# Kernel optimization log

Measured on AMD Instinct MI355X. Metric: run time of the kernel, lower is better.

The kernel has to match this reference:

```python
import jax, jax.numpy as jnp
import numpy as np

B, D, TC, TE, TGT = 8, 256, 2048, 2048, 256
SCALE = 16.0  # sqrt(256.0) hardcoded in the original module


def setup_inputs() -> dict:
    key = jax.random.key(0)
    k1, k2, k3 = jax.random.split(key, 3)
    content_emb = jax.random.normal(k1, (B, D, TC), dtype=jnp.float32)
    emotion_emb = jax.random.normal(k2, (B, D, TE), dtype=jnp.float32)
    # Conv1d(embed_dim*2 -> target_embed, kernel=3): weight [out, in, k]
    fan_in = 2 * D * 3
    conv_w = jax.random.normal(k3, (TGT, 2 * D, 3), dtype=jnp.float32) / np.sqrt(fan_in)
    conv_b = jnp.zeros((TGT,), dtype=jnp.float32)
    return {"content_emb": content_emb, "emotion_emb": emotion_emb,
            "conv_w": conv_w, "conv_b": conv_b}


def reference(content_emb, emotion_emb, conv_w, conv_b):
    # (B, D, T) -> (B, T, D)
    c = jnp.transpose(content_emb, (0, 2, 1))   # [B, Tc, D]
    e = jnp.transpose(emotion_emb, (0, 2, 1))   # [B, Te, D]
    sim = jnp.einsum('btd,bsd->bts', c, e)      # [B, Tc, Te]
    attn = jax.nn.softmax(sim / SCALE, axis=-1)
    weighted_emo = jnp.einsum('bts,bsd->btd', attn, e)  # [B, Tc, D]
    x = jnp.concatenate([c, weighted_emo], axis=-1)     # [B, Tc, 2D]
    x = jnp.transpose(x, (0, 2, 1))                     # [B, 2D, Tc]
    out = jax.lax.conv_general_dilated(
        x, conv_w, window_strides=(1,), padding=[(1, 1)],
        dimension_numbers=('NCH', 'OIH', 'NCH'))
    return out + conv_b[None, :, None]
```

## Files before the change

### kernel.cpp

```cpp
#include <hip/hip_runtime.h>

typedef __bf16 bf16x8 __attribute__((ext_vector_type(8)));
typedef __bf16 bf16x4 __attribute__((ext_vector_type(4)));
typedef float  f32x4  __attribute__((ext_vector_type(4)));

#define MFMA(a, b, c) __builtin_amdgcn_mfma_f32_16x16x32_bf16((a), (b), (c), 0, 0, 0)
#define DRAIN_VMCNT() __builtin_amdgcn_s_waitcnt(0x0F70)

constexpr int Bc  = 8;
constexpr int D   = 256;
constexpr int TC  = 2048;
constexpr int TE  = 2048;
constexpr int TGT = 256;
constexpr int XR  = 512;
constexpr int CROW = 520;
constexpr int NBT = Bc * TC;

#define EXP_C 0.09016844005556021f

__device__ __forceinline__ void gl_lds16(const __bf16* g, __bf16* l) {
  __builtin_amdgcn_global_load_lds(
      (const __attribute__((address_space(1))) void*)g,
      (__attribute__((address_space(3))) void*)l, 16, 0, 0);
}

__global__ void k_transpose_f(const float* __restrict__ src, __bf16* __restrict__ dst,
                              int T, int rowStride) {
  __shared__ __bf16 tile[64][68];
  const int b  = blockIdx.z;
  const int t0 = blockIdx.x * 64;
  const int d0 = blockIdx.y * 64;
  const int tid = threadIdx.x;
  const int c4 = (tid & 15) * 4;
  const int r0 = tid >> 4;
  const float* sp = src + ((size_t)b * D + d0) * T + t0;
#pragma unroll
  for (int i = 0; i < 4; ++i) {
    const int r = r0 + 16 * i;
    const float4 v = *(const float4*)(sp + (size_t)r * T + c4);
    bf16x4 wv;
    wv[0] = (__bf16)v.x; wv[1] = (__bf16)v.y; wv[2] = (__bf16)v.z; wv[3] = (__bf16)v.w;
    *(bf16x4*)&tile[r][c4] = wv;
  }
  __syncthreads();
  __bf16* dp = dst + ((size_t)b * T + t0) * rowStride + d0;
#pragma unroll
  for (int i = 0; i < 2; ++i) {
    const int idx = tid + 256 * i;
    const int r   = idx >> 3;
    const int c8  = (idx & 7) * 8;
    bf16x8 v;
#pragma unroll
    for (int j = 0; j < 8; ++j) v[j] = tile[c8 + j][r];
    *(bf16x8*)(dp + (size_t)r * rowStride + c8) = v;
  }
}

__global__ void k_prep_emo(const float* __restrict__ src, __bf16* __restrict__ e_t,
                           __bf16* __restrict__ e_ds) {
  __shared__ __bf16 tile[64][68];
  const int b  = blockIdx.z;
  const int t0 = blockIdx.x * 64;
  const int d0 = blockIdx.y * 64;
  const int tid = threadIdx.x;
  const int c4 = (tid & 15) * 4;
  const int r0 = tid >> 4;
  const float* sp = src + ((size_t)b * D + d0) * TE + t0;
  __bf16* dsp = e_ds + ((size_t)b * D + d0) * TE + t0;
#pragma unroll
  for (int i = 0; i < 4; ++i) {
    const int r = r0 + 16 * i;
    const float4 v = *(const float4*)(sp + (size_t)r * TE + c4);
    bf16x4 wv;
    wv[0] = (__bf16)v.x; wv[1] = (__bf16)v.y; wv[2] = (__bf16)v.z; wv[3] = (__bf16)v.w;
    *(bf16x4*)&tile[r][c4] = wv;
    *(bf16x4*)(dsp + (size_t)r * TE + c4) = wv;
  }
  __syncthreads();
  __bf16* dp = e_t + ((size_t)b * TE + t0) * D + d0;
#pragma unroll
  for (int i = 0; i < 2; ++i) {
    const int idx = tid + 256 * i;
    const int r   = idx >> 3;
    const int c8  = (idx & 7) * 8;
    bf16x8 v;
#pragma unroll
    for (int j = 0; j < 8; ++j) v[j] = tile[c8 + j][r];
    *(bf16x8*)(dp + (size_t)r * D + c8) = v;
  }
}

__global__ void k_wpack_f(const float* __restrict__ w, __bf16* __restrict__ Wk) {
  const int idx = blockIdx.x * 256 + threadIdx.x;
  const int o = idx >> 9, i = idx & 511;
#pragma unroll
  for (int k = 0; k < 3; ++k)
    Wk[k * (TGT * 512) + idx] = (__bf16)w[(size_t)o * 1536 + i * 3 + k];
}

__global__ __launch_bounds__(256, 2) void k_attn(const __bf16* __restrict__ xcat,
                                                 const __bf16* __restrict__ e_t,
                                                 const __bf16* __restrict__ e_ds,
                                                 __bf16* __restrict__ Op,
                                                 float* __restrict__ Lp) {
  __shared__ __align__(16) __bf16 sEt[2][8192];
  __shared__ __align__(16) __bf16 sEs[2][8192];
  __shared__ __align__(16) __bf16 sP[4][2][640];

  const int tid  = threadIdx.x;
  const int lane = tid & 63;
  const int w    = tid >> 6;
  const int q    = lane >> 4;
  const int tl   = lane & 15;
  const int b    = blockIdx.y;
  const int z    = blockIdx.z;
  const int tbase = blockIdx.x * 128 + w * 32;

  const __bf16* etb = e_t  + (size_t)b * TE * D;
  const __bf16* esb = e_ds + (size_t)b * D * TE;

  bf16x8 cB[2][8];
#pragma unroll
  for (int tt = 0; tt < 2; ++tt) {
    const __bf16* crow = xcat + ((size_t)(b * TC) + tbase + tt * 16 + tl) * XR + q * 8;
#pragma unroll
    for (int ks = 0; ks < 8; ++ks) cB[tt][ks] = *(const bf16x8*)(crow + ks * 32);
  }

  unsigned offEt[4], offEs[4];
#pragma unroll
  for (int c = 0; c < 4; ++c) {
    const int id = (w * 4 + c) * 64 + lane;
    const int ss = id >> 5, cs = id & 31;
    offEt[c] = ss * D + (cs ^ (ss & 7)) * 8;
    const int dd = id >> 2, ps = id & 3;
    offEs[c] = dd * TE + (ps ^ ((dd >> 2) & 3)) * 8;
  }

  f32x4 accO[2][16];
#pragma unroll
  for (int tt = 0; tt < 2; ++tt)
#pragma unroll
    for (int dt = 0; dt < 16; ++dt) accO[tt][dt] = (f32x4){0.f, 0.f, 0.f, 0.f};
  float lacc[2] = {0.f, 0.f};

  const int sbase = z * (TE / 4);
  const int sw3 = (tl >> 2) & 3;

  auto stage = [&](int buf, int s0) {
#pragma unroll
    for (int c = 0; c < 4; ++c) {
      gl_lds16(etb + (size_t)s0 * D + offEt[c], &sEt[buf][(w * 4 + c) * 512]);
      gl_lds16(esb + s0 + offEs[c], &sEs[buf][(w * 4 + c) * 512]);
    }
  };

  stage(0, sbase);
  DRAIN_VMCNT();
  __syncthreads();

  int cur = 0;
  for (int k = 0; k < TE / 128; ++k) {
    if (k < TE / 128 - 1) stage(cur ^ 1, sbase + (k + 1) * 32);

    f32x4 aS[2][2];
#pragma unroll
    for (int i = 0; i < 2; ++i)
#pragma unroll
      for (int j = 0; j < 2; ++j) aS[i][j] = (f32x4){0.f, 0.f, 0.f, 0.f};
    const __bf16* pe = &sEt[cur][0];
    __builtin_amdgcn_s_setprio(1);
#pragma unroll
    for (int ks = 0; ks < 8; ++ks) {
      const int ch = (ks * 4 + q) ^ (tl & 7);
      bf16x8 a0 = *(const bf16x8*)(pe + (tl * 32 + ch) * 8);
      bf16x8 a1 = *(const bf16x8*)(pe + ((16 + tl) * 32 + ch) * 8);
      aS[0][0] = MFMA(a0, cB[0][ks], aS[0][0]);
      aS[0][1] = MFMA(a0, cB[1][ks], aS[0][1]);
      aS[1][0] = MFMA(a1, cB[0][ks], aS[1][0]);
      aS[1][1] = MFMA(a1, cB[1][ks], aS[1][1]);
    }
    __builtin_amdgcn_s_setprio(0);

#pragma unroll
    for (int tt = 0; tt < 2; ++tt) {
      bf16x4 w0, w1;
#pragma unroll
      for (int r = 0; r < 4; ++r) {
        float e0 = exp2f(aS[0][tt][r] * EXP_C);
        float e1 = exp2f(aS[1][tt][r] * EXP_C);
        lacc[tt] += e0 + e1;
        w0[r] = (__bf16)e0;
        w1[r] = (__bf16)e1;
      }
      __bf16* pw = &sP[w][tt][tl * 40 + q * 4];
      *(bf16x4*)pw = w0;
      *(bf16x4*)(pw + 16) = w1;
    }
    bf16x8 pB0 = *(const bf16x8*)(&sP[w][0][tl * 40 + q * 8]);
    bf16x8 pB1 = *(const bf16x8*)(&sP[w][1][tl * 40 + q * 8]);

    const __bf16* ps = &sEs[cur][0];
    __builtin_amdgcn_s_setprio(1);
#pragma unroll
    for (int dt = 0; dt < 16; ++dt) {
      bf16x8 a = *(const bf16x8*)(ps + ((dt * 16 + tl) * 4 + (q ^ sw3)) * 8);
      accO[0][dt] = MFMA(a, pB0, accO[0][dt]);
      accO[1][dt] = MFMA(a, pB1, accO[1][dt]);
    }
    __builtin_amdgcn_s_setprio(0);

    DRAIN_VMCNT();
    __syncthreads();
    cur ^= 1;
  }

#pragma unroll
  for (int tt = 0; tt < 2; ++tt) {
    float v = lacc[tt];
    v += __shfl_xor(v, 16, 64);
    v += __shfl_xor(v, 32, 64);
    const size_t row = (size_t)z * NBT + b * TC + tbase + tt * 16 + tl;
    if (q == 0) Lp[row] = v;
    __bf16* orow = Op + row * D + q * 4;
#pragma unroll
    for (int dt = 0; dt < 16; ++dt) {
      bf16x4 o;
#pragma unroll
      for (int r = 0; r < 4; ++r) o[r] = (__bf16)accO[tt][dt][r];
      *(bf16x4*)(orow + dt * 16) = o;
    }
  }
}

__global__ void k_norm(const __bf16* __restrict__ Op, const float* __restrict__ Lp,
                       __bf16* __restrict__ xcat) {
  const int row  = blockIdx.x * 4 + (threadIdx.x >> 6);
  const int lane = threadIdx.x & 63;
  float lsum = 0.f;
#pragma unroll
  for (int zz = 0; zz < 4; ++zz) lsum += Lp[zz * NBT + row];
  const float inv = 1.0f / lsum;
  float acc[4] = {0.f, 0.f, 0.f, 0.f};
#pragma unroll
  for (int zz = 0; zz < 4; ++zz) {
    bf16x4 a = *(const bf16x4*)(Op + ((size_t)zz * NBT + row) * D + lane * 4);
#pragma unroll
    for (int r = 0; r < 4; ++r) acc[r] += (float)a[r];
  }
  bf16x4 o;
#pragma unroll
  for (int r = 0; r < 4; ++r) o[r] = (__bf16)(acc[r] * inv);
  *(bf16x4*)(xcat + (size_t)row * XR + D + lane * 4) = o;
}

__global__ __launch_bounds__(256, 2) void k_conv(const __bf16* __restrict__ xcat,
                                                 const __bf16* __restrict__ Wk,
                                                 const float* __restrict__ bias,
                                                 float* __restrict__ out) {
  __shared__ __align__(16) __bf16 sX[34 * CROW];
  __shared__ __align__(16) __bf16 sW[2][8192];
  const int tid  = threadIdx.x;
  const int lane = tid & 63;
  const int wv   = tid >> 6;
  const int q    = lane >> 4;
  const int tl   = lane & 15;
  const int b    = blockIdx.x & 7;
  const int t0   = (blockIdx.x >> 3) * 32;
  const int o0   = wv * 64;
  const int sw3  = (tl >> 2) & 3;

  const __bf16* xb = xcat + (size_t)b * TC * XR;
  for (int r = wv; r < 34; r += 4) {
    int gr = t0 - 1 + r;
    gr = gr < 0 ? 0 : (gr > TC - 1 ? TC - 1 : gr);
    gl_lds16(xb + (size_t)gr * XR + lane * 8, &sX[r * CROW]);
  }

  unsigned offW[4];
#pragma unroll
  for (int c = 0; c < 4; ++c) {
    const int id = (wv * 4 + c) * 64 + lane;
    const int o = id >> 2, ps = id & 3;
    offW[c] = o * 512 + (ps ^ ((o >> 2) & 3)) * 8;
  }
  auto stageW = [&](int buf, int s) {
    const int kk = s >> 4, is = s & 15;
    const __bf16* wb = Wk + (size_t)kk * TGT * 512 + is * 32;
#pragma unroll
    for (int c = 0; c < 4; ++c)
      gl_lds16(wb + offW[c], &sW[buf][(wv * 4 + c) * 512]);
  };
  stageW(0, 0);
  DRAIN_VMCNT();
  __syncthreads();
  if (t0 == 0)       for (int i = tid; i < CROW; i += 256) sX[i] = (__bf16)0.f;
  if (t0 + 32 == TC) for (int i = tid; i < CROW; i += 256) sX[33 * CROW + i] = (__bf16)0.f;
  __syncthreads();

  f32x4 acc[4][2];
#pragma unroll
  for (int mt = 0; mt < 4; ++mt) {
#pragma unroll
    for (int r = 0; r < 4; ++r) {
      const float bv = bias[o0 + mt * 16 + q * 4 + r];
#pragma unroll
      for (int nt = 0; nt < 2; ++nt) acc[mt][nt][r] = bv;
    }
  }

  int cur = 0;
  for (int s = 0; s < 48; ++s) {
    if (s < 47) stageW(cur ^ 1, s + 1);
    const int kk = s >> 4, is = s & 15;
    bf16x8 bfr[2];
#pragma unroll
    for (int nt = 0; nt < 2; ++nt)
      bfr[nt] = *(const bf16x8*)(&sX[(nt * 16 + tl + kk) * CROW + is * 32 + q * 8]);
    __builtin_amdgcn_s_setprio(1);
#pragma unroll
    for (int mt = 0; mt < 4; ++mt) {
      const int o = o0 + mt * 16 + tl;
      bf16x8 af = *(const bf16x8*)(&sW[cur][(o * 4 + (q ^ sw3)) * 8]);
#pragma unroll
      for (int nt = 0; nt < 2; ++nt) acc[mt][nt] = MFMA(af, bfr[nt], acc[mt][nt]);
    }
    __builtin_amdgcn_s_setprio(0);
    DRAIN_VMCNT();
    __syncthreads();
    cur ^= 1;
  }

#pragma unroll
  for (int mt = 0; mt < 4; ++mt) {
#pragma unroll
    for (int nt = 0; nt < 2; ++nt) {
#pragma unroll
      for (int r = 0; r < 4; ++r) {
        const int o = o0 + mt * 16 + q * 4 + r;
        const int t = t0 + nt * 16 + tl;
        out[((size_t)b * TGT + o) * TC + t] = acc[mt][nt][r];
      }
    }
  }
}

extern "C" void kernel_launch(void* const* d_in, const int* in_sizes, int n_in,
                              void* d_out, int out_size, void* d_ws, size_t ws_size,
                              hipStream_t stream) {
  (void)in_sizes; (void)n_in; (void)out_size; (void)ws_size;
  const float* content = (const float*)d_in[0];
  const float* emotion = (const float*)d_in[1];
  const float* conv_w  = (const float*)d_in[2];
  const float* conv_b  = (const float*)d_in[3];
  float* out = (float*)d_out;

  char* ws = (char*)d_ws;
  __bf16* xcat = (__bf16*)ws;
  __bf16* Wk   = (__bf16*)(ws + 16777216);
  __bf16* Op   = (__bf16*)(ws + 17563648);
  float*  Lp   = (float*)(ws + 51118080);
  __bf16* e_t  = (__bf16*)d_out;
  __bf16* e_ds = (__bf16*)((char*)d_out + 8388608);

  k_transpose_f<<<dim3(TC / 64, D / 64, Bc), 256, 0, stream>>>(content, xcat, TC, XR);
  k_prep_emo<<<dim3(TE / 64, D / 64, Bc), 256, 0, stream>>>(emotion, e_t, e_ds);
  k_wpack_f<<<512, 256, 0, stream>>>(conv_w, Wk);
  k_attn<<<dim3(TC / 128, Bc, 4), 256, 0, stream>>>(xcat, e_t, e_ds, Op, Lp);
  k_norm<<<NBT / 4, 256, 0, stream>>>(Op, Lp, xcat);
  k_conv<<<dim3((TC / 32) * Bc), 256, 0, stream>>>(xcat, Wk, conv_b, out);
}
```

Baseline: 185.9 us.

## Fuse prep kernels into one and fold split-K normalization into conv staging

```diff
diff --git a/kernel.cpp b/kernel.cpp
--- a/kernel.cpp
+++ b/kernel.cpp
@@ -12,8 +12,7 @@
 constexpr int TC  = 2048;
 constexpr int TE  = 2048;
 constexpr int TGT = 256;
-constexpr int XR  = 512;
-constexpr int CROW = 520;
+constexpr int XR  = 256;
 constexpr int NBT = Bc * TC;
 
 #define EXP_C 0.09016844005556021f
@@ -24,26 +23,47 @@
       (__attribute__((address_space(3))) void*)l, 16, 0, 0);
 }
 
-__global__ void k_transpose_f(const float* __restrict__ src, __bf16* __restrict__ dst,
-                              int T, int rowStride) {
+__global__ void k_prep_all(const float* __restrict__ content,
+                           const float* __restrict__ emotion,
+                           __bf16* __restrict__ xcat,
+                           __bf16* __restrict__ e_t, __bf16* __restrict__ e_ds,
+                           const float* __restrict__ w, __bf16* __restrict__ Wk) {
   __shared__ __bf16 tile[64][68];
+  const int tid = threadIdx.x;
+
+  if (blockIdx.x == TC / 64) {
+    const int base = (blockIdx.y * Bc + blockIdx.z) * 2048;
+#pragma unroll
+    for (int j = 0; j < 8; ++j) {
+      const int idx = base + j * 256 + tid;
+      const int o = idx >> 9, i = idx & 511;
+#pragma unroll
+      for (int k = 0; k < 3; ++k)
+        Wk[k * (TGT * 512) + idx] = (__bf16)w[(size_t)o * 1536 + i * 3 + k];
+    }
+    return;
+  }
+
+  const bool isC = blockIdx.y < 4;
   const int b  = blockIdx.z;
   const int t0 = blockIdx.x * 64;
-  const int d0 = blockIdx.y * 64;
-  const int tid = threadIdx.x;
+  const int d0 = (blockIdx.y & 3) * 64;
   const int c4 = (tid & 15) * 4;
   const int r0 = tid >> 4;
-  const float* sp = src + ((size_t)b * D + d0) * T + t0;
+  const float* sp = (isC ? content : emotion) + ((size_t)b * D + d0) * 2048 + t0;
+  __bf16* dsp = e_ds + ((size_t)b * D + d0) * TE + t0;
 #pragma unroll
   for (int i = 0; i < 4; ++i) {
     const int r = r0 + 16 * i;
-    const float4 v = *(const float4*)(sp + (size_t)r * T + c4);
-    bf16x4 wv;
-    wv[0] = (__bf16)v.x; wv[1] = (__bf16)v.y; wv[2] = (__bf16)v.z; wv[3] = (__bf16)v.w;
-    *(bf16x4*)&tile[r][c4] = wv;
+    const float4 v = *(const float4*)(sp + (size_t)r * 2048 + c4);
+    bf16x4 pv;
+    pv[0] = (__bf16)v.x; pv[1] = (__bf16)v.y; pv[2] = (__bf16)v.z; pv[3] = (__bf16)v.w;
+    *(bf16x4*)&tile[r][c4] = pv;
+    if (!isC) *(bf16x4*)(dsp + (size_t)r * TE + c4) = pv;
   }
   __syncthreads();
-  __bf16* dp = dst + ((size_t)b * T + t0) * rowStride + d0;
+  __bf16* dp = (isC ? xcat + ((size_t)b * TC + t0) * XR
+                    : e_t + ((size_t)b * TE + t0) * D) + d0;
 #pragma unroll
   for (int i = 0; i < 2; ++i) {
     const int idx = tid + 256 * i;
@@ -52,50 +72,8 @@
     bf16x8 v;
 #pragma unroll
     for (int j = 0; j < 8; ++j) v[j] = tile[c8 + j][r];
-    *(bf16x8*)(dp + (size_t)r * rowStride + c8) = v;
-  }
-}
-
-__global__ void k_prep_emo(const float* __restrict__ src, __bf16* __restrict__ e_t,
-                           __bf16* __restrict__ e_ds) {
-  __shared__ __bf16 tile[64][68];
-  const int b  = blockIdx.z;
-  const int t0 = blockIdx.x * 64;
-  const int d0 = blockIdx.y * 64;
-  const int tid = threadIdx.x;
-  const int c4 = (tid & 15) * 4;
-  const int r0 = tid >> 4;
-  const float* sp = src + ((size_t)b * D + d0) * TE + t0;
-  __bf16* dsp = e_ds + ((size_t)b * D + d0) * TE + t0;
-#pragma unroll
-  for (int i = 0; i < 4; ++i) {
-    const int r = r0 + 16 * i;
-    const float4 v = *(const float4*)(sp + (size_t)r * TE + c4);
-    bf16x4 wv;
-    wv[0] = (__bf16)v.x; wv[1] = (__bf16)v.y; wv[2] = (__bf16)v.z; wv[3] = (__bf16)v.w;
-    *(bf16x4*)&tile[r][c4] = wv;
-    *(bf16x4*)(dsp + (size_t)r * TE + c4) = wv;
-  }
-  __syncthreads();
-  __bf16* dp = e_t + ((size_t)b * TE + t0) * D + d0;
-#pragma unroll
-  for (int i = 0; i < 2; ++i) {
-    const int idx = tid + 256 * i;
-    const int r   = idx >> 3;
-    const int c8  = (idx & 7) * 8;
-    bf16x8 v;
-#pragma unroll
-    for (int j = 0; j < 8; ++j) v[j] = tile[c8 + j][r];
-    *(bf16x8*)(dp + (size_t)r * D + c8) = v;
-  }
-}
-
-__global__ void k_wpack_f(const float* __restrict__ w, __bf16* __restrict__ Wk) {
-  const int idx = blockIdx.x * 256 + threadIdx.x;
-  const int o = idx >> 9, i = idx & 511;
-#pragma unroll
-  for (int k = 0; k < 3; ++k)
-    Wk[k * (TGT * 512) + idx] = (__bf16)w[(size_t)o * 1536 + i * 3 + k];
+    *(bf16x8*)(dp + (size_t)r * 256 + c8) = v;
+  }
 }
 
 __global__ __launch_bounds__(256, 2) void k_attn(const __bf16* __restrict__ xcat,
@@ -169,7 +147,6 @@
 #pragma unroll
       for (int j = 0; j < 2; ++j) aS[i][j] = (f32x4){0.f, 0.f, 0.f, 0.f};
     const __bf16* pe = &sEt[cur][0];
-    __builtin_amdgcn_s_setprio(1);
 #pragma unroll
     for (int ks = 0; ks < 8; ++ks) {
       const int ch = (ks * 4 + q) ^ (tl & 7);
@@ -180,7 +157,6 @@
       aS[1][0] = MFMA(a1, cB[0][ks], aS[1][0]);
       aS[1][1] = MFMA(a1, cB[1][ks], aS[1][1]);
     }
-    __builtin_amdgcn_s_setprio(0);
 
 #pragma unroll
     for (int tt = 0; tt < 2; ++tt) {
@@ -201,14 +177,12 @@
     bf16x8 pB1 = *(const bf16x8*)(&sP[w][1][tl * 40 + q * 8]);
 
     const __bf16* ps = &sEs[cur][0];
-    __builtin_amdgcn_s_setprio(1);
 #pragma unroll
     for (int dt = 0; dt < 16; ++dt) {
       bf16x8 a = *(const bf16x8*)(ps + ((dt * 16 + tl) * 4 + (q ^ sw3)) * 8);
       accO[0][dt] = MFMA(a, pB0, accO[0][dt]);
       accO[1][dt] = MFMA(a, pB1, accO[1][dt]);
     }
-    __builtin_amdgcn_s_setprio(0);
 
     DRAIN_VMCNT();
     __syncthreads();
@@ -233,32 +207,14 @@
   }
 }
 
-__global__ void k_norm(const __bf16* __restrict__ Op, const float* __restrict__ Lp,
-                       __bf16* __restrict__ xcat) {
-  const int row  = blockIdx.x * 4 + (threadIdx.x >> 6);
-  const int lane = threadIdx.x & 63;
-  float lsum = 0.f;
-#pragma unroll
-  for (int zz = 0; zz < 4; ++zz) lsum += Lp[zz * NBT + row];
-  const float inv = 1.0f / lsum;
-  float acc[4] = {0.f, 0.f, 0.f, 0.f};
-#pragma unroll
-  for (int zz = 0; zz < 4; ++zz) {
-    bf16x4 a = *(const bf16x4*)(Op + ((size_t)zz * NBT + row) * D + lane * 4);
-#pragma unroll
-    for (int r = 0; r < 4; ++r) acc[r] += (float)a[r];
-  }
-  bf16x4 o;
-#pragma unroll
-  for (int r = 0; r < 4; ++r) o[r] = (__bf16)(acc[r] * inv);
-  *(bf16x4*)(xcat + (size_t)row * XR + D + lane * 4) = o;
-}
-
 __global__ __launch_bounds__(256, 2) void k_conv(const __bf16* __restrict__ xcat,
+                                                 const __bf16* __restrict__ Op,
+                                                 const float* __restrict__ Lp,
                                                  const __bf16* __restrict__ Wk,
                                                  const float* __restrict__ bias,
                                                  float* __restrict__ out) {
-  __shared__ __align__(16) __bf16 sX[34 * CROW];
+  __shared__ __align__(16) __bf16 sXA[34 * 256];
+  __shared__ __align__(16) __bf16 sXB[34 * 256];
   __shared__ __align__(16) __bf16 sW[2][8192];
   const int tid  = threadIdx.x;
   const int lane = tid & 63;
@@ -269,12 +225,16 @@
   const int t0   = (blockIdx.x >> 3) * 32;
   const int o0   = wv * 64;
   const int sw3  = (tl >> 2) & 3;
+  const int rh   = lane >> 5;
+  const int l5   = lane & 31;
 
   const __bf16* xb = xcat + (size_t)b * TC * XR;
-  for (int r = wv; r < 34; r += 4) {
-    int gr = t0 - 1 + r;
+  for (int i = wv; i < 17; i += 4) {
+    const int rl = 2 * i + rh;
+    int gr = t0 - 1 + rl;
     gr = gr < 0 ? 0 : (gr > TC - 1 ? TC - 1 : gr);
-    gl_lds16(xb + (size_t)gr * XR + lane * 8, &sX[r * CROW]);
+    const int cs = l5 ^ (rl & 7);
+    gl_lds16(xb + (size_t)gr * XR + cs * 8, &sXA[i * 512]);
   }
 
   unsigned offW[4];
@@ -292,11 +252,38 @@
       gl_lds16(wb + offW[c], &sW[buf][(wv * 4 + c) * 512]);
   };
   stageW(0, 0);
+
+  for (int i = wv; i < 17; i += 4) {
+    const int rl = 2 * i + rh;
+    int gr = t0 - 1 + rl;
+    gr = gr < 0 ? 0 : (gr > TC - 1 ? TC - 1 : gr);
+    const size_t row = (size_t)b * TC + gr;
+    const float inv = 1.0f /
+        (Lp[row] + Lp[NBT + row] + Lp[2 * NBT + row] + Lp[3 * NBT + row]);
+    float a8[8] = {0.f, 0.f, 0.f, 0.f, 0.f, 0.f, 0.f, 0.f};
+#pragma unroll
+    for (int zz = 0; zz < 4; ++zz) {
+      bf16x8 a = *(const bf16x8*)(Op + ((size_t)zz * NBT + row) * D + l5 * 8);
+#pragma unroll
+      for (int r = 0; r < 8; ++r) a8[r] += (float)a[r];
+    }
+    bf16x8 o;
+#pragma unroll
+    for (int r = 0; r < 8; ++r) o[r] = (__bf16)(a8[r] * inv);
+    *(bf16x8*)((char*)&sXB[rl * 256] + ((l5 * 16) ^ ((rl & 7) << 4))) = o;
+  }
+
   DRAIN_VMCNT();
   __syncthreads();
-  if (t0 == 0)       for (int i = tid; i < CROW; i += 256) sX[i] = (__bf16)0.f;
-  if (t0 + 32 == TC) for (int i = tid; i < CROW; i += 256) sX[33 * CROW + i] = (__bf16)0.f;
-  __syncthreads();
+
+  if (t0 == 0) {
+    sXA[tid] = (__bf16)0.f; sXB[tid] = (__bf16)0.f;
+    __syncthreads();
+  }
+  if (t0 + 32 == TC) {
+    sXA[33 * 256 + tid] = (__bf16)0.f; sXB[33 * 256 + tid] = (__bf16)0.f;
+    __syncthreads();
+  }
 
   f32x4 acc[4][2];
 #pragma unroll
@@ -313,11 +300,14 @@
   for (int s = 0; s < 48; ++s) {
     if (s < 47) stageW(cur ^ 1, s + 1);
     const int kk = s >> 4, is = s & 15;
+    const __bf16* pl = (is & 8) ? sXB : sXA;
+    const int cbyte = (is & 7) * 64 + q * 16;
     bf16x8 bfr[2];
 #pragma unroll
-    for (int nt = 0; nt < 2; ++nt)
-      bfr[nt] = *(const bf16x8*)(&sX[(nt * 16 + tl + kk) * CROW + is * 32 + q * 8]);
-    __builtin_amdgcn_s_setprio(1);
+    for (int nt = 0; nt < 2; ++nt) {
+      const int t = nt * 16 + tl + kk;
+      bfr[nt] = *(const bf16x8*)((const char*)pl + t * 512 + (cbyte ^ ((t & 7) << 4)));
+    }
 #pragma unroll
     for (int mt = 0; mt < 4; ++mt) {
       const int o = o0 + mt * 16 + tl;
@@ -325,7 +315,6 @@
 #pragma unroll
       for (int nt = 0; nt < 2; ++nt) acc[mt][nt] = MFMA(af, bfr[nt], acc[mt][nt]);
     }
-    __builtin_amdgcn_s_setprio(0);
     DRAIN_VMCNT();
     __syncthreads();
     cur ^= 1;
@@ -357,16 +346,14 @@
 
   char* ws = (char*)d_ws;
   __bf16* xcat = (__bf16*)ws;
-  __bf16* Wk   = (__bf16*)(ws + 16777216);
-  __bf16* Op   = (__bf16*)(ws + 17563648);
-  float*  Lp   = (float*)(ws + 51118080);
+  __bf16* Wk   = (__bf16*)(ws + 8388608);
+  __bf16* Op   = (__bf16*)(ws + 9437184);
+  float*  Lp   = (float*)(ws + 42991616);
   __bf16* e_t  = (__bf16*)d_out;
   __bf16* e_ds = (__bf16*)((char*)d_out + 8388608);
 
-  k_transpose_f<<<dim3(TC / 64, D / 64, Bc), 256, 0, stream>>>(content, xcat, TC, XR);
-  k_prep_emo<<<dim3(TE / 64, D / 64, Bc), 256, 0, stream>>>(emotion, e_t, e_ds);
-  k_wpack_f<<<512, 256, 0, stream>>>(conv_w, Wk);
+  k_prep_all<<<dim3(TC / 64 + 1, 8, Bc), 256, 0, stream>>>(
+      content, emotion, xcat, e_t, e_ds, conv_w, Wk);
   k_attn<<<dim3(TC / 128, Bc, 4), 256, 0, stream>>>(xcat, e_t, e_ds, Op, Lp);
-  k_norm<<<NBT / 4, 256, 0, stream>>>(Op, Lp, xcat);
-  k_conv<<<dim3((TC / 32) * Bc), 256, 0, stream>>>(xcat, Wk, conv_b, out);
-}
+  k_conv<<<dim3((TC / 32) * Bc), 256, 0, stream>>>(xcat, Op, Lp, Wk, conv_b, out);
+}
```

New measurement: 179.3 us. 3.6% less time.
